# Kernel tuning notes

Hardware: AMD Instinct MI355X
Metric: run time of the kernel (lower is better)

Reference implementation:

```python
import jax, jax.numpy as jnp
import numpy as np
from jax import lax

MODEL_DIM = 384
KERNEL = 15
PAD = (KERNEL - 1) // 2
BATCH = 4096


def fake_quant(x, bits):
    """Per-tensor symmetric fake quantization with straight-through estimator.
    scale = max|x| / qmax, q = clip(round(x/scale), qmin, qmax), dq = q*scale.
    """
    qmax = float(2 ** (bits - 1) - 1)
    qmin = -float(2 ** (bits - 1))
    scale = jnp.maximum(jnp.max(jnp.abs(x)) / qmax, jnp.asarray(1e-8, x.dtype))
    dq = jnp.clip(jnp.round(x / scale), qmin, qmax) * scale
    return x + lax.stop_gradient(dq - x)  # STE: identity gradient


def setup_inputs() -> dict:
    key = jax.random.key(0)
    k = jax.random.split(key, 7)
    image = jax.random.normal(k[0], (BATCH, 28, 28), dtype=jnp.float32)
    # LinearQuant(28 -> model_dim)
    W1 = jax.random.normal(k[1], (MODEL_DIM, 28), dtype=jnp.float32) * (1.0 / np.sqrt(28))
    b1 = jax.random.normal(k[2], (MODEL_DIM,), dtype=jnp.float32) * 0.01
    # depthwise Conv1DQuant(model_dim, model_dim, K, groups=model_dim): weight [C_out, 1, K]
    Wc = jax.random.normal(k[3], (MODEL_DIM, 1, KERNEL), dtype=jnp.float32) * (1.0 / np.sqrt(KERNEL))
    bc = jax.random.normal(k[4], (MODEL_DIM,), dtype=jnp.float32) * 0.01
    # LinearQuant(28*model_dim -> 10)
    Wf = jax.random.normal(k[5], (10, 28 * MODEL_DIM), dtype=jnp.float32) * (1.0 / np.sqrt(28 * MODEL_DIM))
    bf = jax.random.normal(k[6], (10,), dtype=jnp.float32) * 0.01
    return {"image": image, "W1": W1, "b1": b1, "Wc": Wc, "bc": bc, "Wf": Wf, "bf": bf}


def reference(image, W1, b1, Wc, bc, Wf, bf):
    inp = image.reshape(-1, 28, 28)
    # linear_1 with 8-bit activation fake-quant in and 3-bit weight fake-quant
    x = fake_quant(inp, 8)
    lin = jnp.einsum('blf,of->blo', x, fake_quant(W1, 3)) + b1  # [B,28,model_dim]
    out1 = jnp.tanh(fake_quant(lin, 8))
    # depthwise conv1d over length 28, channels model_dim
    xc = jnp.transpose(fake_quant(out1, 8), (0, 2, 1))  # [B,C,L]
    conv = lax.conv_general_dilated(
        xc, fake_quant(Wc, 3), window_strides=(1,), padding=[(PAD, PAD)],
        dimension_numbers=('NCH', 'OIH', 'NCH'), feature_group_count=MODEL_DIM)
    conv = conv + bc[None, :, None]                      # [B,C,L]
    conv = jnp.transpose(conv, (0, 2, 1))                # [B,L,C]
    out2 = jnp.tanh(fake_quant(conv, 8)).reshape(-1, MODEL_DIM * 28)
    # final linear
    logits = fake_quant(out2, 8) @ fake_quant(Wf, 3).T + bf  # [B,10]
    return fake_quant(logits, 8)
```

## Files before the change

kernel.cpp:

```cpp
#include <hip/hip_runtime.h>

#define BATCH 4096
#define MD 384
#define KW 15
#define LSEQ 28
#define FIN 28
#define NX (BATCH*LSEQ*FIN)
#define NROWS (BATCH*LSEQ)

#define B_SCF  0
#define B_LUT1 256
#define B_LUT2 512
#define B_PT0  1024
#define B_PT1  33792
#define B_PT2  50176
#define B_PTL  66560
#define B_W1B  74752
#define B_WCQ  99328
#define B_WFB  105472
#define B_LG   277504
#define B_XQB  441344
#define B_CWG  7781376

typedef __bf16 bf16x8 __attribute__((ext_vector_type(8)));
typedef float f32x4 __attribute__((ext_vector_type(4)));
typedef int i32x4 __attribute__((ext_vector_type(4)));

#if __has_builtin(__builtin_amdgcn_sdot4)
#define SDOT4(a,b,c) __builtin_amdgcn_sdot4((a),(b),(c),false)
#else
__device__ __forceinline__ int SDOT4(int a,int b,int c){
  c += ((a<<24)>>24)*((b<<24)>>24);
  c += ((a<<16)>>24)*((b<<16)>>24);
  c += ((a<<8)>>24)*((b<<8)>>24);
  c += (a>>24)*(b>>24);
  return c;
}
#endif

#if __has_builtin(__builtin_amdgcn_alignbyte)
#define ALIGNB(hi,lo,s) __builtin_amdgcn_alignbyte((hi),(lo),(s))
#else
#define ALIGNB(hi,lo,s) ((int)(((unsigned)(lo)>>(8*(s)))|((unsigned)(hi)<<(32-8*(s)))))
#endif

__device__ __forceinline__ unsigned short f2bf(float f){
  return (unsigned short)(__float_as_uint(f)>>16);
}
__device__ __forceinline__ unsigned lut_bperm(int iw,int lutw){
  int res=__builtin_amdgcn_ds_bpermute(iw,lutw);
  return ((unsigned)res>>(8*(iw&3)))&0xFFu;
}

__device__ __forceinline__ void blkStore4(float m0,float m1,float m2,float m3,float4* dst){
  #pragma unroll
  for(int off=32;off;off>>=1){
    m0=fmaxf(m0,__shfl_xor(m0,off,64));
    m1=fmaxf(m1,__shfl_xor(m1,off,64));
    m2=fmaxf(m2,__shfl_xor(m2,off,64));
    m3=fmaxf(m3,__shfl_xor(m3,off,64));
  }
  __shared__ float sm[4][4];
  int wid=threadIdx.x>>6;
  if((threadIdx.x&63)==0){sm[wid][0]=m0;sm[wid][1]=m1;sm[wid][2]=m2;sm[wid][3]=m3;}
  __syncthreads();
  if(threadIdx.x==0){
    for(int i=1;i<4;i++){
      m0=fmaxf(m0,sm[i][0]);m1=fmaxf(m1,sm[i][1]);
      m2=fmaxf(m2,sm[i][2]);m3=fmaxf(m3,sm[i][3]);
    }
    *dst=make_float4(m0,m1,m2,m3);
  }
}

__device__ __forceinline__ void blkStoreMM(float mn,float mx,float2* dst){
  #pragma unroll
  for(int off=32;off;off>>=1){
    mn=fminf(mn,__shfl_xor(mn,off,64));
    mx=fmaxf(mx,__shfl_xor(mx,off,64));
  }
  __shared__ float smn[8],smx[8];
  int wid=threadIdx.x>>6, nw=blockDim.x>>6;
  if((threadIdx.x&63)==0){smn[wid]=mn;smx[wid]=mx;}
  __syncthreads();
  if(threadIdx.x==0){
    for(int i=1;i<nw;i++){mn=fminf(mn,smn[i]);mx=fmaxf(mx,smx[i]);}
    *dst=make_float2(mn,mx);
  }
}

__global__ __launch_bounds__(256)
void k_maxabs_in(const float* __restrict__ img,const float* __restrict__ W1,
                 const float* __restrict__ Wc,const float* __restrict__ Wf,
                 float4* __restrict__ pt0){
  float m0=0.f,m1=0.f,m2=0.f,m3=0.f;
  const int N4=NX/4;
  const int NW1=MD*FIN, NWC=MD*KW, NWF=10*MD*LSEQ;
  const int total=N4+NW1+NWC+NWF;
  const float4* img4=(const float4*)img;
  for(int i=blockIdx.x*blockDim.x+threadIdx.x;i<total;i+=gridDim.x*blockDim.x){
    if(i<N4){
      float4 v=img4[i];
      m0=fmaxf(m0,fmaxf(fmaxf(fabsf(v.x),fabsf(v.y)),fmaxf(fabsf(v.z),fabsf(v.w))));
    }
    else if(i<N4+NW1) m1=fmaxf(m1,fabsf(W1[i-N4]));
    else if(i<N4+NW1+NWC) m2=fmaxf(m2,fabsf(Wc[i-N4-NW1]));
    else m3=fmaxf(m3,fabsf(Wf[i-N4-NW1-NWC]));
  }
  blkStore4(m0,m1,m2,m3,&pt0[blockIdx.x]);
}

__global__ __launch_bounds__(256)
void k_prep(const float* __restrict__ img,const float* __restrict__ W1,
            const float* __restrict__ Wc,const float* __restrict__ Wf,
            const float4* __restrict__ pt0,float* __restrict__ scf,
            char* __restrict__ wsb){
  int t=threadIdx.x;
  float m0=0.f,m1=0.f,m2=0.f,m3=0.f;
  for(int i=t;i<2048;i+=256){
    float4 v=pt0[i];
    m0=fmaxf(m0,v.x);m1=fmaxf(m1,v.y);m2=fmaxf(m2,v.z);m3=fmaxf(m3,v.w);
  }
  #pragma unroll
  for(int off=32;off;off>>=1){
    m0=fmaxf(m0,__shfl_xor(m0,off,64));
    m1=fmaxf(m1,__shfl_xor(m1,off,64));
    m2=fmaxf(m2,__shfl_xor(m2,off,64));
    m3=fmaxf(m3,__shfl_xor(m3,off,64));
  }
  __shared__ float sm[4][4];
  __shared__ float bsv[4];
  int wid=t>>6;
  if((t&63)==0){sm[wid][0]=m0;sm[wid][1]=m1;sm[wid][2]=m2;sm[wid][3]=m3;}
  __syncthreads();
  if(t==0){
    for(int i=1;i<4;i++){
      m0=fmaxf(m0,sm[i][0]);m1=fmaxf(m1,sm[i][1]);
      m2=fmaxf(m2,sm[i][2]);m3=fmaxf(m3,sm[i][3]);
    }
    bsv[0]=fmaxf(m0/127.f,1e-8f);
    bsv[1]=fmaxf(m1/3.f,1e-8f);
    bsv[2]=fmaxf(m2/3.f,1e-8f);
    bsv[3]=fmaxf(m3/3.f,1e-8f);
    if(blockIdx.x==0){scf[0]=bsv[0];scf[1]=bsv[1];scf[2]=bsv[2];scf[3]=bsv[3];}
  }
  __syncthreads();
  float s_img=bsv[0], s_w1=bsv[1], s_wc=bsv[2], s_wf=bsv[3];
  float inv_img=1.f/s_img;
  unsigned short* xqb=(unsigned short*)(wsb+B_XQB);
  unsigned short* w1b=(unsigned short*)(wsb+B_W1B);
  char* wcpk=wsb+B_WCQ;
  char* wfb=wsb+B_WFB;
  const int T0=NROWS*32;
  const int T1=T0+MD*32;
  const int T2=T1+MD*16;
  const int T3=T2+10*10752;
  for(int i=blockIdx.x*blockDim.x+threadIdx.x;i<T3;i+=gridDim.x*blockDim.x){
    if(i<T0){
      int row=i>>5, cc=i&31;
      float q = cc<FIN ? fminf(fmaxf(rintf(img[row*FIN+cc]*inv_img),-128.f),127.f) : 0.f;
      xqb[i]=f2bf(q);
    } else if(i<T1){
      int j=i-T0; int o=j>>5, cc=j&31;
      float q = cc<FIN ? fminf(fmaxf(rintf(W1[o*FIN+cc]/s_w1),-4.f),3.f) : 0.f;
      w1b[j]=f2bf(q);
    } else if(i<T2){
      int j=i-T1; int c=j>>4, k=j&15;
      char q=0;
      if(k<KW) q=(char)(int)fminf(fmaxf(rintf(Wc[c*KW+k]/s_wc),-4.f),3.f);
      wcpk[j]=q;
    } else {
      int j=i-T2;
      int n=j/10752, r=j-n*10752;
      int c=r/28, l=r-c*28;
      wfb[j]=(char)(int)fminf(fmaxf(rintf(Wf[n*10752+l*MD+c]/s_wf),-4.f),3.f);
    }
  }
}

__global__ __launch_bounds__(256)
void k_redmm(const float2* __restrict__ pt,int n,float* __restrict__ scf,
             int preIdx,int outIdx,char* __restrict__ lutg){
  int t=threadIdx.x;
  float mn=1e30f,mx=-1e30f;
  for(int i=t;i<n;i+=256){
    float2 v=pt[i];
    mn=fminf(mn,v.x); mx=fmaxf(mx,v.y);
  }
  #pragma unroll
  for(int off=32;off;off>>=1){
    mn=fminf(mn,__shfl_xor(mn,off,64));
    mx=fmaxf(mx,__shfl_xor(mx,off,64));
  }
  __shared__ float smn[4],smx[4];
  __shared__ float bs,bso;
  int wid=t>>6;
  if((t&63)==0){smn[wid]=mn;smx[wid]=mx;}
  __syncthreads();
  if(t==0){
    for(int i=1;i<4;i++){mn=fminf(mn,smn[i]);mx=fmaxf(mx,smx[i]);}
    float ma=fmaxf(fabsf(mn),fabsf(mx));
    float s=fmaxf(ma/127.f,1e-8f);
    float a1=fabsf(fminf(fmaxf(rintf(mn/s),-128.f),127.f)*s);
    float a2=fabsf(fminf(fmaxf(rintf(mx/s),-128.f),127.f)*s);
    float so=fmaxf(tanhf(fmaxf(a1,a2))/127.f,1e-8f);
    scf[preIdx]=s; scf[outIdx]=so;
    bs=s; bso=so;
  }
  __syncthreads();
  float d=(float)(t-128)*bs;
  lutg[t]=(char)(int)fminf(fmaxf(rintf(tanhf(d)/bso),-128.f),127.f);
}

#define CWS 29
#define DWS 2692
template<int MODE>
__global__ __launch_bounds__(512)
void k_fused(const unsigned short* __restrict__ xqb,const unsigned short* __restrict__ w1b,
             const float* __restrict__ b1,const float* __restrict__ scf,
             const char* __restrict__ lut1g,const char* __restrict__ lut2g,
             const char* __restrict__ wcpk,const float* __restrict__ bc,
             const char* __restrict__ wfb,const float* __restrict__ bfv,
             int* __restrict__ cwg,
             float2* __restrict__ ptmm,float* __restrict__ lg,
             float* __restrict__ ptl){
  __shared__ int ldsI[MD*CWS];
  __shared__ int psumN[8][10][4];
  int t=threadIdx.x, wid=t>>6, lane=t&63, l4=lane>>4, l15=lane&15;

  bf16x8 bfr[3]; float b1v[3]; bf16x8 af[7];
  if constexpr(MODE<2){
    const int* src=(const int*)w1b;
    for(int i=t;i<6144;i+=512) ldsI[i]=src[i];
    __syncthreads();
    unsigned short* Wlds=(unsigned short*)ldsI;
    #pragma unroll
    for(int ni=0;ni<3;ni++){
      int o=(wid*3+ni)*16+l15;
      bfr[ni]=*(const bf16x8*)&Wlds[o*32+l4*8];
      b1v[ni]=b1[o];
    }
    int r0=blockIdx.x*112;
    #pragma unroll
    for(int mt=0;mt<7;mt++)
      af[mt]=*(const bf16x8*)&xqb[(size_t)(r0+mt*16+l15)*32+l4*8];
  } else {
    const int4* src=(const int4*)(cwg+(size_t)blockIdx.x*10752);
    for(int jj=t;jj<2688;jj+=512){
      int4 v=src[jj];
      int j=jj*4, o=j/28, idx=j-o*28, base=o*CWS+idx;
      ldsI[base]=v.x; ldsI[base+1]=v.y; ldsI[base+2]=v.z; ldsI[base+3]=v.w;
    }
  }

  float sg=scf[0]*scf[1];
  float sgi=sg, b1s[3]={0.f,0.f,0.f};
  int lutA_w=0,lutB_w=0;
  float ck1=1.f,inv_cv=1.f,sfac=1.f,gsc=1.f;
  if constexpr(MODE>=1){
    sfac=scf[5]*scf[2];
  }
  if constexpr(MODE==1){
    float inv_lin=1.f/scf[4];
    sgi=sg*inv_lin;
    #pragma unroll
    for(int ni=0;ni<3;ni++) b1s[ni]=fmaf(b1v[ni],inv_lin,128.f);
    lutA_w=((const int*)lut1g)[lane];
  }
  if constexpr(MODE==2){
    inv_cv=1.f/scf[6];
    ck1=sfac*inv_cv;
    gsc=scf[3]*scf[7];
    lutB_w=((const int*)lut2g)[lane];
  }
  if constexpr(MODE>=1) __syncthreads();

  if constexpr(MODE<2){
    f32x4 zero={0.f,0.f,0.f,0.f};
    float mnn[3]={1e30f,1e30f,1e30f},mxx[3]={-1e30f,-1e30f,-1e30f};
    #pragma unroll
    for(int ni=0;ni<3;ni++){
      int o=(wid*3+ni)*16+l15;
      #pragma unroll
      for(int mt=0;mt<7;mt++){
        f32x4 acc=__builtin_amdgcn_mfma_f32_16x16x32_bf16(af[mt],bfr[ni],zero,0,0,0);
        if constexpr(MODE==0){
          #pragma unroll
          for(int r=0;r<4;r++){
            mnn[ni]=fminf(mnn[ni],acc[r]); mxx[ni]=fmaxf(mxx[ni],acc[r]);
          }
        } else {
          unsigned w=0;
          #pragma unroll
          for(int r=0;r<4;r++){
            float x=fmaf(acc[r],sgi,b1s[ni]);
            int iw=(int)__builtin_amdgcn_fmed3f(rintf(x),0.f,255.f);
            w|=lut_bperm(iw,lutA_w)<<(8*r);
          }
          ldsI[o*CWS+mt*4+l4]=(int)w;
        }
      }
    }
    if constexpr(MODE==0){
      float mn=1e30f,mx=-1e30f;
      #pragma unroll
      for(int ni=0;ni<3;ni++){
        mn=fminf(mn,fmaf(mnn[ni],sg,b1v[ni]));
        mx=fmaxf(mx,fmaf(mxx[ni],sg,b1v[ni]));
      }
      blkStoreMM(mn,mx,&ptmm[blockIdx.x]);
      return;
    }
    __syncthreads();
    {
      int4* dst=(int4*)(cwg+(size_t)blockIdx.x*10752);
      for(int jj=t;jj<2688;jj+=512){
        int j=jj*4, o=j/28, idx=j-o*28, base=o*CWS+idx;
        int4 v; v.x=ldsI[base]; v.y=ldsI[base+1]; v.z=ldsI[base+2]; v.w=ldsI[base+3];
        dst[jj]=v;
      }
    }
  }

  int oww[3][7];
  float mnc=1e30f,mxc=-1e30f;
  #pragma unroll
  for(int rr=0;rr<3;rr++){
    int j=t+rr*512;
    int s=j/384, c=j-s*384;
    i32x4 wq=*(const i32x4*)(wcpk+(size_t)c*16);
    float cbias=bc[c];
    float cq2=0.f;
    if constexpr(MODE==2) cq2=fmaf(cbias,inv_cv,128.f);
    int ext[11];
    ext[0]=0; ext[1]=0; ext[9]=0; ext[10]=0;
    #pragma unroll
    for(int i=0;i<7;i++) ext[2+i]=ldsI[c*CWS+s*7+i];
    int imn=0x7FFFFFFF,imx=0x80000000;
    #pragma unroll
    for(int l=0;l<LSEQ;l++){
      const int eb=l+1, bi=eb>>2, sh=eb&3;
      int A0,A1,A2,A3;
      if(sh==0){A0=ext[bi];A1=ext[bi+1];A2=ext[bi+2];A3=ext[bi+3];}
      else{
        A0=ALIGNB(ext[bi+1],ext[bi],sh);
        A1=ALIGNB(ext[bi+2],ext[bi+1],sh);
        A2=ALIGNB(ext[bi+3],ext[bi+2],sh);
        A3=ALIGNB(ext[bi+4],ext[bi+3],sh);
      }
      int idot=SDOT4(A0,wq[0],SDOT4(A1,wq[1],SDOT4(A2,wq[2],SDOT4(A3,wq[3],0))));
      if constexpr(MODE==1){
        imn=min(imn,idot); imx=max(imx,idot);
      } else {
        float x=fmaf((float)idot,ck1,cq2);
        int iw=(int)__builtin_amdgcn_fmed3f(rintf(x),0.f,255.f);
        unsigned q2=lut_bperm(iw,lutB_w);
        if((l&3)==0) oww[rr][l>>2]=(int)q2;
        else oww[rr][l>>2]|=(int)(q2<<(8*(l&3)));
      }
    }
    if constexpr(MODE==1){
      mnc=fminf(mnc,fmaf((float)imn,sfac,cbias));
      mxc=fmaxf(mxc,fmaf((float)imx,sfac,cbias));
    }
  }
  if constexpr(MODE==1){
    blkStoreMM(mnc,mxc,&ptmm[blockIdx.x]);
    return;
  }

  __syncthreads();
  #pragma unroll
  for(int rr=0;rr<3;rr++){
    int j=t+rr*512;
    int s=j/384, c=j-s*384;
    #pragma unroll
    for(int i=0;i<7;i++) ldsI[s*DWS+c*7+i]=oww[rr][i];
  }
  __syncthreads();

  {
    i32x4 acc0={0,0,0,0}, acc1={0,0,0,0};
    const char* ldsB=(const char*)ldsI;
    for(int kb=wid;kb<168;kb+=16){
      i32x4 a=*(const i32x4*)(ldsB+(size_t)(l15&3)*(DWS*4)+kb*64+l4*16);
      i32x4 b=*(const i32x4*)(wfb+(size_t)l15*10752+kb*64+l4*16);
      acc0=__builtin_amdgcn_mfma_i32_16x16x64_i8(a,b,acc0,0,0,0);
      int kb2=kb+8;
      if(kb2<168){
        i32x4 a2=*(const i32x4*)(ldsB+(size_t)(l15&3)*(DWS*4)+kb2*64+l4*16);
        i32x4 b2=*(const i32x4*)(wfb+(size_t)l15*10752+kb2*64+l4*16);
        acc1=__builtin_amdgcn_mfma_i32_16x16x64_i8(a2,b2,acc1,0,0,0);
      }
    }
    if(l4==0&&l15<10){
      #pragma unroll
      for(int r=0;r<4;r++) psumN[wid][l15][r]=acc0[r]+acc1[r];
    }
  }
  __syncthreads();
  float m=0.f;
  if(t<40){
    int s=t/10, o=t-s*10;
    int sum=0;
    #pragma unroll
    for(int w=0;w<8;w++) sum+=psumN[w][o][s];
    float v=fmaf((float)sum,gsc,bfv[o]);
    lg[(blockIdx.x*4+s)*10+o]=v;
    m=fabsf(v);
  }
  if(t<64){
    #pragma unroll
    for(int off=32;off;off>>=1) m=fmaxf(m,__shfl_xor(m,off,64));
    if(t==0) ptl[blockIdx.x]=m;
  }
}

__global__ __launch_bounds__(256)
void k_final(const float* __restrict__ lg,const float* __restrict__ ptl,
             float* __restrict__ out){
  int t=threadIdx.x;
  float m=0.f;
  for(int i=t;i<1024;i+=256) m=fmaxf(m,ptl[i]);
  #pragma unroll
  for(int off=32;off;off>>=1) m=fmaxf(m,__shfl_xor(m,off,64));
  __shared__ float sm[4];
  __shared__ float sv;
  int wid=t>>6;
  if((t&63)==0) sm[wid]=m;
  __syncthreads();
  if(t==0){
    for(int k=1;k<4;k++) m=fmaxf(m,sm[k]);
    sv=fmaxf(m/127.f,1e-8f);
  }
  __syncthreads();
  float s=sv;
  int i=blockIdx.x*256+t;
  out[i]=fminf(fmaxf(rintf(lg[i]/s),-128.f),127.f)*s;
}

extern "C" void kernel_launch(void* const* d_in, const int* in_sizes, int n_in,
                              void* d_out, int out_size, void* d_ws, size_t ws_size,
                              hipStream_t stream){
  const float* img=(const float*)d_in[0];
  const float* W1 =(const float*)d_in[1];
  const float* b1 =(const float*)d_in[2];
  const float* Wc =(const float*)d_in[3];
  const float* bc =(const float*)d_in[4];
  const float* Wf =(const float*)d_in[5];
  const float* bf =(const float*)d_in[6];
  float* out=(float*)d_out;
  char* wsb=(char*)d_ws;
  float* scf=(float*)(wsb+B_SCF);
  float4* pt0=(float4*)(wsb+B_PT0);
  float2* pt1=(float2*)(wsb+B_PT1);
  float2* pt2=(float2*)(wsb+B_PT2);
  float* ptl=(float*)(wsb+B_PTL);
  float* lg=(float*)(wsb+B_LG);
  int* cwg=(int*)(wsb+B_CWG);
  const unsigned short* xqb=(const unsigned short*)(wsb+B_XQB);
  const unsigned short* w1b=(const unsigned short*)(wsb+B_W1B);
  const char* wcpk=wsb+B_WCQ;
  const char* wfb=wsb+B_WFB;

  k_maxabs_in<<<2048,256,0,stream>>>(img,W1,Wc,Wf,pt0);
  k_prep<<<2048,256,0,stream>>>(img,W1,Wc,Wf,pt0,scf,wsb);
  k_fused<0><<<1024,512,0,stream>>>(xqb,w1b,b1,scf,nullptr,nullptr,wcpk,bc,wfb,bf,cwg,pt1,nullptr,nullptr);
  k_redmm<<<1,256,0,stream>>>(pt1,1024,scf,4,5,wsb+B_LUT1);
  k_fused<1><<<1024,512,0,stream>>>(xqb,w1b,b1,scf,wsb+B_LUT1,nullptr,wcpk,bc,wfb,bf,cwg,pt2,nullptr,nullptr);
  k_redmm<<<1,256,0,stream>>>(pt2,1024,scf,6,7,wsb+B_LUT2);
  k_fused<2><<<1024,512,0,stream>>>(xqb,w1b,b1,scf,wsb+B_LUT1,wsb+B_LUT2,wcpk,bc,wfb,bf,cwg,nullptr,lg,ptl);
  k_final<<<160,256,0,stream>>>(lg,ptl,out);
}
```

Measured before the change: 105.8 us.

## Merge all stages into one cooperative persistent kernel with grid syncs

Replaces the eight separate launches (maxabs, prep, three fused passes, two reductions, final) with a single cooperative kernel. Grid-wide barriers separate the stages, each block loops over tiles persistently, and the scale reductions and tanh lookup tables are recomputed per block in shared memory. This removes launch gaps and the single-block reduction kernels. In exchange the grid is capped at co-resident blocks (at most 512), each block processes multiple tiles serially, and each grid sync costs a global barrier.

```diff
diff --git a/kernel.cpp b/kernel.cpp
--- a/kernel.cpp
+++ b/kernel.cpp
@@ -1,4 +1,6 @@
 #include <hip/hip_runtime.h>
+#include <hip/hip_cooperative_groups.h>
+namespace cg = cooperative_groups;
 
 #define BATCH 4096
 #define MD 384
@@ -7,10 +9,8 @@
 #define FIN 28
 #define NX (BATCH*LSEQ*FIN)
 #define NROWS (BATCH*LSEQ)
-
-#define B_SCF  0
-#define B_LUT1 256
-#define B_LUT2 512
+#define NTILE 1024
+
 #define B_PT0  1024
 #define B_PT1  33792
 #define B_PT2  50176
@@ -52,184 +52,131 @@
   return ((unsigned)res>>(8*(iw&3)))&0xFFu;
 }
 
-__device__ __forceinline__ void blkStore4(float m0,float m1,float m2,float m3,float4* dst){
-  #pragma unroll
-  for(int off=32;off;off>>=1){
-    m0=fmaxf(m0,__shfl_xor(m0,off,64));
-    m1=fmaxf(m1,__shfl_xor(m1,off,64));
-    m2=fmaxf(m2,__shfl_xor(m2,off,64));
-    m3=fmaxf(m3,__shfl_xor(m3,off,64));
-  }
-  __shared__ float sm[4][4];
-  int wid=threadIdx.x>>6;
-  if((threadIdx.x&63)==0){sm[wid][0]=m0;sm[wid][1]=m1;sm[wid][2]=m2;sm[wid][3]=m3;}
-  __syncthreads();
-  if(threadIdx.x==0){
-    for(int i=1;i<4;i++){
-      m0=fmaxf(m0,sm[i][0]);m1=fmaxf(m1,sm[i][1]);
-      m2=fmaxf(m2,sm[i][2]);m3=fmaxf(m3,sm[i][3]);
-    }
-    *dst=make_float4(m0,m1,m2,m3);
-  }
-}
-
-__device__ __forceinline__ void blkStoreMM(float mn,float mx,float2* dst){
-  #pragma unroll
-  for(int off=32;off;off>>=1){
-    mn=fminf(mn,__shfl_xor(mn,off,64));
-    mx=fmaxf(mx,__shfl_xor(mx,off,64));
-  }
-  __shared__ float smn[8],smx[8];
-  int wid=threadIdx.x>>6, nw=blockDim.x>>6;
-  if((threadIdx.x&63)==0){smn[wid]=mn;smx[wid]=mx;}
-  __syncthreads();
-  if(threadIdx.x==0){
-    for(int i=1;i<nw;i++){mn=fminf(mn,smn[i]);mx=fmaxf(mx,smx[i]);}
-    *dst=make_float2(mn,mx);
-  }
-}
-
-__global__ __launch_bounds__(256)
-void k_maxabs_in(const float* __restrict__ img,const float* __restrict__ W1,
-                 const float* __restrict__ Wc,const float* __restrict__ Wf,
-                 float4* __restrict__ pt0){
-  float m0=0.f,m1=0.f,m2=0.f,m3=0.f;
-  const int N4=NX/4;
-  const int NW1=MD*FIN, NWC=MD*KW, NWF=10*MD*LSEQ;
-  const int total=N4+NW1+NWC+NWF;
-  const float4* img4=(const float4*)img;
-  for(int i=blockIdx.x*blockDim.x+threadIdx.x;i<total;i+=gridDim.x*blockDim.x){
-    if(i<N4){
-      float4 v=img4[i];
-      m0=fmaxf(m0,fmaxf(fmaxf(fabsf(v.x),fabsf(v.y)),fmaxf(fabsf(v.z),fabsf(v.w))));
-    }
-    else if(i<N4+NW1) m1=fmaxf(m1,fabsf(W1[i-N4]));
-    else if(i<N4+NW1+NWC) m2=fmaxf(m2,fabsf(Wc[i-N4-NW1]));
-    else m3=fmaxf(m3,fabsf(Wf[i-N4-NW1-NWC]));
-  }
-  blkStore4(m0,m1,m2,m3,&pt0[blockIdx.x]);
-}
-
-__global__ __launch_bounds__(256)
-void k_prep(const float* __restrict__ img,const float* __restrict__ W1,
-            const float* __restrict__ Wc,const float* __restrict__ Wf,
-            const float4* __restrict__ pt0,float* __restrict__ scf,
-            char* __restrict__ wsb){
-  int t=threadIdx.x;
-  float m0=0.f,m1=0.f,m2=0.f,m3=0.f;
-  for(int i=t;i<2048;i+=256){
-    float4 v=pt0[i];
-    m0=fmaxf(m0,v.x);m1=fmaxf(m1,v.y);m2=fmaxf(m2,v.z);m3=fmaxf(m3,v.w);
-  }
-  #pragma unroll
-  for(int off=32;off;off>>=1){
-    m0=fmaxf(m0,__shfl_xor(m0,off,64));
-    m1=fmaxf(m1,__shfl_xor(m1,off,64));
-    m2=fmaxf(m2,__shfl_xor(m2,off,64));
-    m3=fmaxf(m3,__shfl_xor(m3,off,64));
-  }
-  __shared__ float sm[4][4];
-  __shared__ float bsv[4];
-  int wid=t>>6;
-  if((t&63)==0){sm[wid][0]=m0;sm[wid][1]=m1;sm[wid][2]=m2;sm[wid][3]=m3;}
-  __syncthreads();
-  if(t==0){
-    for(int i=1;i<4;i++){
-      m0=fmaxf(m0,sm[i][0]);m1=fmaxf(m1,sm[i][1]);
-      m2=fmaxf(m2,sm[i][2]);m3=fmaxf(m3,sm[i][3]);
-    }
-    bsv[0]=fmaxf(m0/127.f,1e-8f);
-    bsv[1]=fmaxf(m1/3.f,1e-8f);
-    bsv[2]=fmaxf(m2/3.f,1e-8f);
-    bsv[3]=fmaxf(m3/3.f,1e-8f);
-    if(blockIdx.x==0){scf[0]=bsv[0];scf[1]=bsv[1];scf[2]=bsv[2];scf[3]=bsv[3];}
-  }
-  __syncthreads();
-  float s_img=bsv[0], s_w1=bsv[1], s_wc=bsv[2], s_wf=bsv[3];
-  float inv_img=1.f/s_img;
+#define CWS 29
+#define DWS 2692
+
+__global__ __launch_bounds__(512,4)
+void k_mega(const float* __restrict__ img,const float* __restrict__ W1v,
+            const float* __restrict__ b1,const float* __restrict__ Wc,
+            const float* __restrict__ bc,const float* __restrict__ Wf,
+            const float* __restrict__ bfv,float* __restrict__ out,
+            char* __restrict__ wsb,int nblk){
+  cg::grid_group grid=cg::this_grid();
+  __shared__ int ldsI[MD*CWS];
+  __shared__ int psumN[8][10][4];
+  __shared__ char lutA[256];
+  __shared__ char lutB[256];
+  __shared__ float sred[8][4];
+  __shared__ float bsv[9];
+
+  int t=threadIdx.x, bid=blockIdx.x;
+  int wid=t>>6, lane=t&63, l4=lane>>4, l15=lane&15;
+
+  float4* pt0=(float4*)(wsb+B_PT0);
+  float2* pt1=(float2*)(wsb+B_PT1);
+  float2* pt2=(float2*)(wsb+B_PT2);
+  float* ptl=(float*)(wsb+B_PTL);
+  float* lg=(float*)(wsb+B_LG);
+  int* cwg=(int*)(wsb+B_CWG);
   unsigned short* xqb=(unsigned short*)(wsb+B_XQB);
   unsigned short* w1b=(unsigned short*)(wsb+B_W1B);
   char* wcpk=wsb+B_WCQ;
   char* wfb=wsb+B_WFB;
-  const int T0=NROWS*32;
-  const int T1=T0+MD*32;
-  const int T2=T1+MD*16;
-  const int T3=T2+10*10752;
-  for(int i=blockIdx.x*blockDim.x+threadIdx.x;i<T3;i+=gridDim.x*blockDim.x){
-    if(i<T0){
-      int row=i>>5, cc=i&31;
-      float q = cc<FIN ? fminf(fmaxf(rintf(img[row*FIN+cc]*inv_img),-128.f),127.f) : 0.f;
-      xqb[i]=f2bf(q);
-    } else if(i<T1){
-      int j=i-T0; int o=j>>5, cc=j&31;
-      float q = cc<FIN ? fminf(fmaxf(rintf(W1[o*FIN+cc]/s_w1),-4.f),3.f) : 0.f;
-      w1b[j]=f2bf(q);
-    } else if(i<T2){
-      int j=i-T1; int c=j>>4, k=j&15;
-      char q=0;
-      if(k<KW) q=(char)(int)fminf(fmaxf(rintf(Wc[c*KW+k]/s_wc),-4.f),3.f);
-      wcpk[j]=q;
-    } else {
-      int j=i-T2;
-      int n=j/10752, r=j-n*10752;
-      int c=r/28, l=r-c*28;
-      wfb[j]=(char)(int)fminf(fmaxf(rintf(Wf[n*10752+l*MD+c]/s_wf),-4.f),3.f);
-    }
-  }
-}
-
-__global__ __launch_bounds__(256)
-void k_redmm(const float2* __restrict__ pt,int n,float* __restrict__ scf,
-             int preIdx,int outIdx,char* __restrict__ lutg){
-  int t=threadIdx.x;
-  float mn=1e30f,mx=-1e30f;
-  for(int i=t;i<n;i+=256){
-    float2 v=pt[i];
-    mn=fminf(mn,v.x); mx=fmaxf(mx,v.y);
-  }
-  #pragma unroll
-  for(int off=32;off;off>>=1){
-    mn=fminf(mn,__shfl_xor(mn,off,64));
-    mx=fmaxf(mx,__shfl_xor(mx,off,64));
-  }
-  __shared__ float smn[4],smx[4];
-  __shared__ float bs,bso;
-  int wid=t>>6;
-  if((t&63)==0){smn[wid]=mn;smx[wid]=mx;}
-  __syncthreads();
-  if(t==0){
-    for(int i=1;i<4;i++){mn=fminf(mn,smn[i]);mx=fmaxf(mx,smx[i]);}
-    float ma=fmaxf(fabsf(mn),fabsf(mx));
-    float s=fmaxf(ma/127.f,1e-8f);
-    float a1=fabsf(fminf(fmaxf(rintf(mn/s),-128.f),127.f)*s);
-    float a2=fabsf(fminf(fmaxf(rintf(mx/s),-128.f),127.f)*s);
-    float so=fmaxf(tanhf(fmaxf(a1,a2))/127.f,1e-8f);
-    scf[preIdx]=s; scf[outIdx]=so;
-    bs=s; bso=so;
-  }
-  __syncthreads();
-  float d=(float)(t-128)*bs;
-  lutg[t]=(char)(int)fminf(fmaxf(rintf(tanhf(d)/bso),-128.f),127.f);
-}
-
-#define CWS 29
-#define DWS 2692
-template<int MODE>
-__global__ __launch_bounds__(512)
-void k_fused(const unsigned short* __restrict__ xqb,const unsigned short* __restrict__ w1b,
-             const float* __restrict__ b1,const float* __restrict__ scf,
-             const char* __restrict__ lut1g,const char* __restrict__ lut2g,
-             const char* __restrict__ wcpk,const float* __restrict__ bc,
-             const char* __restrict__ wfb,const float* __restrict__ bfv,
-             int* __restrict__ cwg,
-             float2* __restrict__ ptmm,float* __restrict__ lg,
-             float* __restrict__ ptl){
-  __shared__ int ldsI[MD*CWS];
-  __shared__ int psumN[8][10][4];
-  int t=threadIdx.x, wid=t>>6, lane=t&63, l4=lane>>4, l15=lane&15;
-
-  bf16x8 bfr[3]; float b1v[3]; bf16x8 af[7];
-  if constexpr(MODE<2){
+
+  {
+    float m0=0.f,m1=0.f,m2=0.f,m3=0.f;
+    const int N4=NX/4;
+    const int NW1=MD*FIN,NWC=MD*KW,NWF=10*MD*LSEQ;
+    const int total=N4+NW1+NWC+NWF;
+    const float4* img4=(const float4*)img;
+    for(int i=bid*512+t;i<total;i+=nblk*512){
+      if(i<N4){
+        float4 v=img4[i];
+        m0=fmaxf(m0,fmaxf(fmaxf(fabsf(v.x),fabsf(v.y)),fmaxf(fabsf(v.z),fabsf(v.w))));
+      }
+      else if(i<N4+NW1) m1=fmaxf(m1,fabsf(W1v[i-N4]));
+      else if(i<N4+NW1+NWC) m2=fmaxf(m2,fabsf(Wc[i-N4-NW1]));
+      else m3=fmaxf(m3,fabsf(Wf[i-N4-NW1-NWC]));
+    }
+    #pragma unroll
+    for(int off=32;off;off>>=1){
+      m0=fmaxf(m0,__shfl_xor(m0,off,64));
+      m1=fmaxf(m1,__shfl_xor(m1,off,64));
+      m2=fmaxf(m2,__shfl_xor(m2,off,64));
+      m3=fmaxf(m3,__shfl_xor(m3,off,64));
+    }
+    if(lane==0){sred[wid][0]=m0;sred[wid][1]=m1;sred[wid][2]=m2;sred[wid][3]=m3;}
+    __syncthreads();
+    if(t==0){
+      for(int i=1;i<8;i++){
+        m0=fmaxf(m0,sred[i][0]);m1=fmaxf(m1,sred[i][1]);
+        m2=fmaxf(m2,sred[i][2]);m3=fmaxf(m3,sred[i][3]);
+      }
+      pt0[bid]=make_float4(m0,m1,m2,m3);
+    }
+    __syncthreads();
+  }
+  grid.sync();
+  {
+    float m0=0.f,m1=0.f,m2=0.f,m3=0.f;
+    for(int i=t;i<nblk;i+=512){
+      float4 v=pt0[i];
+      m0=fmaxf(m0,v.x);m1=fmaxf(m1,v.y);m2=fmaxf(m2,v.z);m3=fmaxf(m3,v.w);
+    }
+    #pragma unroll
+    for(int off=32;off;off>>=1){
+      m0=fmaxf(m0,__shfl_xor(m0,off,64));
+      m1=fmaxf(m1,__shfl_xor(m1,off,64));
+      m2=fmaxf(m2,__shfl_xor(m2,off,64));
+      m3=fmaxf(m3,__shfl_xor(m3,off,64));
+    }
+    if(lane==0){sred[wid][0]=m0;sred[wid][1]=m1;sred[wid][2]=m2;sred[wid][3]=m3;}
+    __syncthreads();
+    if(t==0){
+      for(int i=1;i<8;i++){
+        m0=fmaxf(m0,sred[i][0]);m1=fmaxf(m1,sred[i][1]);
+        m2=fmaxf(m2,sred[i][2]);m3=fmaxf(m3,sred[i][3]);
+      }
+      bsv[0]=fmaxf(m0/127.f,1e-8f);
+      bsv[1]=fmaxf(m1/3.f,1e-8f);
+      bsv[2]=fmaxf(m2/3.f,1e-8f);
+      bsv[3]=fmaxf(m3/3.f,1e-8f);
+    }
+    __syncthreads();
+  }
+  {
+    float s_img=bsv[0],s_w1=bsv[1],s_wc=bsv[2],s_wf=bsv[3];
+    float inv_img=1.f/s_img;
+    const int T0=NROWS*32;
+    const int T1=T0+MD*32;
+    const int T2=T1+MD*16;
+    const int T3=T2+10*10752;
+    for(int i=bid*512+t;i<T3;i+=nblk*512){
+      if(i<T0){
+        int row=i>>5, cc=i&31;
+        float q = cc<FIN ? fminf(fmaxf(rintf(img[row*FIN+cc]*inv_img),-128.f),127.f) : 0.f;
+        xqb[i]=f2bf(q);
+      } else if(i<T1){
+        int j=i-T0; int o=j>>5, cc=j&31;
+        float q = cc<FIN ? fminf(fmaxf(rintf(W1v[o*FIN+cc]/s_w1),-4.f),3.f) : 0.f;
+        w1b[j]=f2bf(q);
+      } else if(i<T2){
+        int j=i-T1; int c=j>>4, k=j&15;
+        char q=0;
+        if(k<KW) q=(char)(int)fminf(fmaxf(rintf(Wc[c*KW+k]/s_wc),-4.f),3.f);
+        wcpk[j]=q;
+      } else {
+        int j=i-T2;
+        int n=j/10752, r=j-n*10752;
+        int c=r/28, l=r-c*28;
+        wfb[j]=(char)(int)fminf(fmaxf(rintf(Wf[n*10752+l*MD+c]/s_wf),-4.f),3.f);
+      }
+    }
+  }
+  grid.sync();
+
+  bf16x8 bfr[3]; float b1v[3];
+  {
     const int* src=(const int*)w1b;
     for(int i=t;i<6144;i+=512) ldsI[i]=src[i];
     __syncthreads();
@@ -240,56 +187,100 @@
       bfr[ni]=*(const bf16x8*)&Wlds[o*32+l4*8];
       b1v[ni]=b1[o];
     }
-    int r0=blockIdx.x*112;
-    #pragma unroll
-    for(int mt=0;mt<7;mt++)
-      af[mt]=*(const bf16x8*)&xqb[(size_t)(r0+mt*16+l15)*32+l4*8];
-  } else {
-    const int4* src=(const int4*)(cwg+(size_t)blockIdx.x*10752);
-    for(int jj=t;jj<2688;jj+=512){
-      int4 v=src[jj];
-      int j=jj*4, o=j/28, idx=j-o*28, base=o*CWS+idx;
-      ldsI[base]=v.x; ldsI[base+1]=v.y; ldsI[base+2]=v.z; ldsI[base+3]=v.w;
-    }
-  }
-
-  float sg=scf[0]*scf[1];
-  float sgi=sg, b1s[3]={0.f,0.f,0.f};
-  int lutA_w=0,lutB_w=0;
-  float ck1=1.f,inv_cv=1.f,sfac=1.f,gsc=1.f;
-  if constexpr(MODE>=1){
-    sfac=scf[5]*scf[2];
-  }
-  if constexpr(MODE==1){
-    float inv_lin=1.f/scf[4];
-    sgi=sg*inv_lin;
-    #pragma unroll
-    for(int ni=0;ni<3;ni++) b1s[ni]=fmaf(b1v[ni],inv_lin,128.f);
-    lutA_w=((const int*)lut1g)[lane];
-  }
-  if constexpr(MODE==2){
-    inv_cv=1.f/scf[6];
-    ck1=sfac*inv_cv;
-    gsc=scf[3]*scf[7];
-    lutB_w=((const int*)lut2g)[lane];
-  }
-  if constexpr(MODE>=1) __syncthreads();
-
-  if constexpr(MODE<2){
+    float sg=bsv[0]*bsv[1];
     f32x4 zero={0.f,0.f,0.f,0.f};
     float mnn[3]={1e30f,1e30f,1e30f},mxx[3]={-1e30f,-1e30f,-1e30f};
-    #pragma unroll
-    for(int ni=0;ni<3;ni++){
-      int o=(wid*3+ni)*16+l15;
-      #pragma unroll
-      for(int mt=0;mt<7;mt++){
-        f32x4 acc=__builtin_amdgcn_mfma_f32_16x16x32_bf16(af[mt],bfr[ni],zero,0,0,0);
-        if constexpr(MODE==0){
+    for(int tile=bid;tile<NTILE;tile+=nblk){
+      bf16x8 af[7];
+      int r0=tile*112;
+      #pragma unroll
+      for(int mt=0;mt<7;mt++)
+        af[mt]=*(const bf16x8*)&xqb[(size_t)(r0+mt*16+l15)*32+l4*8];
+      #pragma unroll
+      for(int ni=0;ni<3;ni++){
+        #pragma unroll
+        for(int mt=0;mt<7;mt++){
+          f32x4 acc=__builtin_amdgcn_mfma_f32_16x16x32_bf16(af[mt],bfr[ni],zero,0,0,0);
           #pragma unroll
           for(int r=0;r<4;r++){
             mnn[ni]=fminf(mnn[ni],acc[r]); mxx[ni]=fmaxf(mxx[ni],acc[r]);
           }
-        } else {
+        }
+      }
+    }
+    float mn=1e30f,mx=-1e30f;
+    #pragma unroll
+    for(int ni=0;ni<3;ni++){
+      mn=fminf(mn,fmaf(mnn[ni],sg,b1v[ni]));
+      mx=fmaxf(mx,fmaf(mxx[ni],sg,b1v[ni]));
+    }
+    #pragma unroll
+    for(int off=32;off;off>>=1){
+      mn=fminf(mn,__shfl_xor(mn,off,64));
+      mx=fmaxf(mx,__shfl_xor(mx,off,64));
+    }
+    if(lane==0){sred[wid][0]=mn;sred[wid][1]=mx;}
+    __syncthreads();
+    if(t==0){
+      for(int i=1;i<8;i++){mn=fminf(mn,sred[i][0]);mx=fmaxf(mx,sred[i][1]);}
+      pt1[bid]=make_float2(mn,mx);
+    }
+    __syncthreads();
+  }
+  grid.sync();
+  {
+    float mn=1e30f,mx=-1e30f;
+    for(int i=t;i<nblk;i+=512){
+      float2 v=pt1[i]; mn=fminf(mn,v.x); mx=fmaxf(mx,v.y);
+    }
+    #pragma unroll
+    for(int off=32;off;off>>=1){
+      mn=fminf(mn,__shfl_xor(mn,off,64));
+      mx=fmaxf(mx,__shfl_xor(mx,off,64));
+    }
+    if(lane==0){sred[wid][0]=mn;sred[wid][1]=mx;}
+    __syncthreads();
+    if(t==0){
+      for(int i=1;i<8;i++){mn=fminf(mn,sred[i][0]);mx=fmaxf(mx,sred[i][1]);}
+      float ma=fmaxf(fabsf(mn),fabsf(mx));
+      float s=fmaxf(ma/127.f,1e-8f);
+      float a1=fabsf(fminf(fmaxf(rintf(mn/s),-128.f),127.f)*s);
+      float a2=fabsf(fminf(fmaxf(rintf(mx/s),-128.f),127.f)*s);
+      bsv[4]=s;
+      bsv[5]=fmaxf(tanhf(fmaxf(a1,a2))/127.f,1e-8f);
+    }
+    __syncthreads();
+    if(t<256){
+      float d=(float)(t-128)*bsv[4];
+      lutA[t]=(char)(int)fminf(fmaxf(rintf(tanhf(d)/bsv[5]),-128.f),127.f);
+    }
+    __syncthreads();
+  }
+
+  {
+    float sg=bsv[0]*bsv[1];
+    float inv_lin=1.f/bsv[4];
+    float sgi=sg*inv_lin;
+    float b1s[3];
+    #pragma unroll
+    for(int ni=0;ni<3;ni++) b1s[ni]=fmaf(b1v[ni],inv_lin,128.f);
+    int lutA_w=((const int*)lutA)[lane];
+    float sfac=bsv[5]*bsv[2];
+    f32x4 zero={0.f,0.f,0.f,0.f};
+    float mnc=1e30f,mxc=-1e30f;
+    for(int tile=bid;tile<NTILE;tile+=nblk){
+      __syncthreads();
+      bf16x8 af[7];
+      int r0=tile*112;
+      #pragma unroll
+      for(int mt=0;mt<7;mt++)
+        af[mt]=*(const bf16x8*)&xqb[(size_t)(r0+mt*16+l15)*32+l4*8];
+      #pragma unroll
+      for(int ni=0;ni<3;ni++){
+        int o=(wid*3+ni)*16+l15;
+        #pragma unroll
+        for(int mt=0;mt<7;mt++){
+          f32x4 acc=__builtin_amdgcn_mfma_f32_16x16x32_bf16(af[mt],bfr[ni],zero,0,0,0);
           unsigned w=0;
           #pragma unroll
           for(int r=0;r<4;r++){
@@ -300,143 +291,200 @@
           ldsI[o*CWS+mt*4+l4]=(int)w;
         }
       }
-    }
-    if constexpr(MODE==0){
-      float mn=1e30f,mx=-1e30f;
-      #pragma unroll
-      for(int ni=0;ni<3;ni++){
-        mn=fminf(mn,fmaf(mnn[ni],sg,b1v[ni]));
-        mx=fmaxf(mx,fmaf(mxx[ni],sg,b1v[ni]));
-      }
-      blkStoreMM(mn,mx,&ptmm[blockIdx.x]);
-      return;
-    }
-    __syncthreads();
-    {
-      int4* dst=(int4*)(cwg+(size_t)blockIdx.x*10752);
-      for(int jj=t;jj<2688;jj+=512){
-        int j=jj*4, o=j/28, idx=j-o*28, base=o*CWS+idx;
-        int4 v; v.x=ldsI[base]; v.y=ldsI[base+1]; v.z=ldsI[base+2]; v.w=ldsI[base+3];
-        dst[jj]=v;
-      }
-    }
-  }
-
-  int oww[3][7];
-  float mnc=1e30f,mxc=-1e30f;
-  #pragma unroll
-  for(int rr=0;rr<3;rr++){
-    int j=t+rr*512;
-    int s=j/384, c=j-s*384;
-    i32x4 wq=*(const i32x4*)(wcpk+(size_t)c*16);
-    float cbias=bc[c];
-    float cq2=0.f;
-    if constexpr(MODE==2) cq2=fmaf(cbias,inv_cv,128.f);
-    int ext[11];
-    ext[0]=0; ext[1]=0; ext[9]=0; ext[10]=0;
-    #pragma unroll
-    for(int i=0;i<7;i++) ext[2+i]=ldsI[c*CWS+s*7+i];
-    int imn=0x7FFFFFFF,imx=0x80000000;
-    #pragma unroll
-    for(int l=0;l<LSEQ;l++){
-      const int eb=l+1, bi=eb>>2, sh=eb&3;
-      int A0,A1,A2,A3;
-      if(sh==0){A0=ext[bi];A1=ext[bi+1];A2=ext[bi+2];A3=ext[bi+3];}
-      else{
-        A0=ALIGNB(ext[bi+1],ext[bi],sh);
-        A1=ALIGNB(ext[bi+2],ext[bi+1],sh);
-        A2=ALIGNB(ext[bi+3],ext[bi+2],sh);
-        A3=ALIGNB(ext[bi+4],ext[bi+3],sh);
-      }
-      int idot=SDOT4(A0,wq[0],SDOT4(A1,wq[1],SDOT4(A2,wq[2],SDOT4(A3,wq[3],0))));
-      if constexpr(MODE==1){
-        imn=min(imn,idot); imx=max(imx,idot);
-      } else {
-        float x=fmaf((float)idot,ck1,cq2);
-        int iw=(int)__builtin_amdgcn_fmed3f(rintf(x),0.f,255.f);
-        unsigned q2=lut_bperm(iw,lutB_w);
-        if((l&3)==0) oww[rr][l>>2]=(int)q2;
-        else oww[rr][l>>2]|=(int)(q2<<(8*(l&3)));
-      }
-    }
-    if constexpr(MODE==1){
-      mnc=fminf(mnc,fmaf((float)imn,sfac,cbias));
-      mxc=fmaxf(mxc,fmaf((float)imx,sfac,cbias));
-    }
-  }
-  if constexpr(MODE==1){
-    blkStoreMM(mnc,mxc,&ptmm[blockIdx.x]);
-    return;
-  }
-
-  __syncthreads();
-  #pragma unroll
-  for(int rr=0;rr<3;rr++){
-    int j=t+rr*512;
-    int s=j/384, c=j-s*384;
-    #pragma unroll
-    for(int i=0;i<7;i++) ldsI[s*DWS+c*7+i]=oww[rr][i];
-  }
-  __syncthreads();
-
-  {
-    i32x4 acc0={0,0,0,0}, acc1={0,0,0,0};
-    const char* ldsB=(const char*)ldsI;
-    for(int kb=wid;kb<168;kb+=16){
-      i32x4 a=*(const i32x4*)(ldsB+(size_t)(l15&3)*(DWS*4)+kb*64+l4*16);
-      i32x4 b=*(const i32x4*)(wfb+(size_t)l15*10752+kb*64+l4*16);
-      acc0=__builtin_amdgcn_mfma_i32_16x16x64_i8(a,b,acc0,0,0,0);
-      int kb2=kb+8;
-      if(kb2<168){
-        i32x4 a2=*(const i32x4*)(ldsB+(size_t)(l15&3)*(DWS*4)+kb2*64+l4*16);
-        i32x4 b2=*(const i32x4*)(wfb+(size_t)l15*10752+kb2*64+l4*16);
-        acc1=__builtin_amdgcn_mfma_i32_16x16x64_i8(a2,b2,acc1,0,0,0);
-      }
-    }
-    if(l4==0&&l15<10){
-      #pragma unroll
-      for(int r=0;r<4;r++) psumN[wid][l15][r]=acc0[r]+acc1[r];
-    }
-  }
-  __syncthreads();
-  float m=0.f;
-  if(t<40){
-    int s=t/10, o=t-s*10;
-    int sum=0;
-    #pragma unroll
-    for(int w=0;w<8;w++) sum+=psumN[w][o][s];
-    float v=fmaf((float)sum,gsc,bfv[o]);
-    lg[(blockIdx.x*4+s)*10+o]=v;
-    m=fabsf(v);
-  }
-  if(t<64){
+      __syncthreads();
+      {
+        int4* dst=(int4*)(cwg+(size_t)tile*10752);
+        for(int jj=t;jj<2688;jj+=512){
+          int j=jj*4, o=j/28, idx=j-o*28, base=o*CWS+idx;
+          int4 v; v.x=ldsI[base]; v.y=ldsI[base+1]; v.z=ldsI[base+2]; v.w=ldsI[base+3];
+          dst[jj]=v;
+        }
+      }
+      #pragma unroll
+      for(int rr=0;rr<3;rr++){
+        int j=t+rr*512;
+        int s=j/384, c=j-s*384;
+        i32x4 wq=*(const i32x4*)(wcpk+(size_t)c*16);
+        float cbias=bc[c];
+        int ext[11];
+        ext[0]=0; ext[1]=0; ext[9]=0; ext[10]=0;
+        #pragma unroll
+        for(int i=0;i<7;i++) ext[2+i]=ldsI[c*CWS+s*7+i];
+        int imn=0x7FFFFFFF,imx=0x80000000;
+        #pragma unroll
+        for(int l=0;l<LSEQ;l++){
+          const int eb=l+1, bi=eb>>2, sh=eb&3;
+          int A0,A1,A2,A3;
+          if(sh==0){A0=ext[bi];A1=ext[bi+1];A2=ext[bi+2];A3=ext[bi+3];}
+          else{
+            A0=ALIGNB(ext[bi+1],ext[bi],sh);
+            A1=ALIGNB(ext[bi+2],ext[bi+1],sh);
+            A2=ALIGNB(ext[bi+3],ext[bi+2],sh);
+            A3=ALIGNB(ext[bi+4],ext[bi+3],sh);
+          }
+          int idot=SDOT4(A0,wq[0],SDOT4(A1,wq[1],SDOT4(A2,wq[2],SDOT4(A3,wq[3],0))));
+          imn=min(imn,idot); imx=max(imx,idot);
+        }
+        mnc=fminf(mnc,fmaf((float)imn,sfac,cbias));
+        mxc=fmaxf(mxc,fmaf((float)imx,sfac,cbias));
+      }
+    }
+    #pragma unroll
+    for(int off=32;off;off>>=1){
+      mnc=fminf(mnc,__shfl_xor(mnc,off,64));
+      mxc=fmaxf(mxc,__shfl_xor(mxc,off,64));
+    }
+    __syncthreads();
+    if(lane==0){sred[wid][0]=mnc;sred[wid][1]=mxc;}
+    __syncthreads();
+    if(t==0){
+      for(int i=1;i<8;i++){mnc=fminf(mnc,sred[i][0]);mxc=fmaxf(mxc,sred[i][1]);}
+      pt2[bid]=make_float2(mnc,mxc);
+    }
+    __syncthreads();
+  }
+  grid.sync();
+  {
+    float mn=1e30f,mx=-1e30f;
+    for(int i=t;i<nblk;i+=512){
+      float2 v=pt2[i]; mn=fminf(mn,v.x); mx=fmaxf(mx,v.y);
+    }
+    #pragma unroll
+    for(int off=32;off;off>>=1){
+      mn=fminf(mn,__shfl_xor(mn,off,64));
+      mx=fmaxf(mx,__shfl_xor(mx,off,64));
+    }
+    if(lane==0){sred[wid][0]=mn;sred[wid][1]=mx;}
+    __syncthreads();
+    if(t==0){
+      for(int i=1;i<8;i++){mn=fminf(mn,sred[i][0]);mx=fmaxf(mx,sred[i][1]);}
+      float ma=fmaxf(fabsf(mn),fabsf(mx));
+      float s=fmaxf(ma/127.f,1e-8f);
+      float a1=fabsf(fminf(fmaxf(rintf(mn/s),-128.f),127.f)*s);
+      float a2=fabsf(fminf(fmaxf(rintf(mx/s),-128.f),127.f)*s);
+      bsv[6]=s;
+      bsv[7]=fmaxf(tanhf(fmaxf(a1,a2))/127.f,1e-8f);
+    }
+    __syncthreads();
+    if(t<256){
+      float d=(float)(t-128)*bsv[6];
+      lutB[t]=(char)(int)fminf(fmaxf(rintf(tanhf(d)/bsv[7]),-128.f),127.f);
+    }
+    __syncthreads();
+  }
+
+  {
+    float inv_cv=1.f/bsv[6];
+    float ck1=bsv[5]*bsv[2]*inv_cv;
+    float gsc=bsv[3]*bsv[7];
+    int lutB_w=((const int*)lutB)[lane];
+    float mL=0.f;
+    for(int tile=bid;tile<NTILE;tile+=nblk){
+      __syncthreads();
+      {
+        const int4* src=(const int4*)(cwg+(size_t)tile*10752);
+        for(int jj=t;jj<2688;jj+=512){
+          int4 v=src[jj];
+          int j=jj*4, o=j/28, idx=j-o*28, base=o*CWS+idx;
+          ldsI[base]=v.x; ldsI[base+1]=v.y; ldsI[base+2]=v.z; ldsI[base+3]=v.w;
+        }
+      }
+      __syncthreads();
+      int oww[3][7];
+      #pragma unroll
+      for(int rr=0;rr<3;rr++){
+        int j=t+rr*512;
+        int s=j/384, c=j-s*384;
+        i32x4 wq=*(const i32x4*)(wcpk+(size_t)c*16);
+        float cq2=fmaf(bc[c],inv_cv,128.f);
+        int ext[11];
+        ext[0]=0; ext[1]=0; ext[9]=0; ext[10]=0;
+        #pragma unroll
+        for(int i=0;i<7;i++) ext[2+i]=ldsI[c*CWS+s*7+i];
+        #pragma unroll
+        for(int l=0;l<LSEQ;l++){
+          const int eb=l+1, bi=eb>>2, sh=eb&3;
+          int A0,A1,A2,A3;
+          if(sh==0){A0=ext[bi];A1=ext[bi+1];A2=ext[bi+2];A3=ext[bi+3];}
+          else{
+            A0=ALIGNB(ext[bi+1],ext[bi],sh);
+            A1=ALIGNB(ext[bi+2],ext[bi+1],sh);
+            A2=ALIGNB(ext[bi+3],ext[bi+2],sh);
+            A3=ALIGNB(ext[bi+4],ext[bi+3],sh);
+          }
+          int idot=SDOT4(A0,wq[0],SDOT4(A1,wq[1],SDOT4(A2,wq[2],SDOT4(A3,wq[3],0))));
+          float x=fmaf((float)idot,ck1,cq2);
+          int iw=(int)__builtin_amdgcn_fmed3f(rintf(x),0.f,255.f);
+          unsigned q2=lut_bperm(iw,lutB_w);
+          if((l&3)==0) oww[rr][l>>2]=(int)q2;
+          else oww[rr][l>>2]|=(int)(q2<<(8*(l&3)));
+        }
+      }
+      __syncthreads();
+      #pragma unroll
+      for(int rr=0;rr<3;rr++){
+        int j=t+rr*512;
+        int s=j/384, c=j-s*384;
+        #pragma unroll
+        for(int i=0;i<7;i++) ldsI[s*DWS+c*7+i]=oww[rr][i];
+      }
+      __syncthreads();
+      {
+        i32x4 acc0={0,0,0,0}, acc1={0,0,0,0};
+        const char* ldsB=(const char*)ldsI;
+        for(int kb=wid;kb<168;kb+=16){
+          i32x4 a=*(const i32x4*)(ldsB+(size_t)(l15&3)*(DWS*4)+kb*64+l4*16);
+          i32x4 b=*(const i32x4*)(wfb+(size_t)l15*10752+kb*64+l4*16);
+          acc0=__builtin_amdgcn_mfma_i32_16x16x64_i8(a,b,acc0,0,0,0);
+          int kb2=kb+8;
+          if(kb2<168){
+            i32x4 a2=*(const i32x4*)(ldsB+(size_t)(l15&3)*(DWS*4)+kb2*64+l4*16);
+            i32x4 b2=*(const i32x4*)(wfb+(size_t)l15*10752+kb2*64+l4*16);
+            acc1=__builtin_amdgcn_mfma_i32_16x16x64_i8(a2,b2,acc1,0,0,0);
+          }
+        }
+        if(l4==0&&l15<10){
+          #pragma unroll
+          for(int r=0;r<4;r++) psumN[wid][l15][r]=acc0[r]+acc1[r];
+        }
+      }
+      __syncthreads();
+      float m=0.f;
+      if(t<40){
+        int s=t/10, o=t-s*10;
+        int sum=0;
+        #pragma unroll
+        for(int w=0;w<8;w++) sum+=psumN[w][o][s];
+        float v=fmaf((float)sum,gsc,bfv[o]);
+        lg[(size_t)tile*40+t]=v;
+        m=fabsf(v);
+      }
+      if(t<64){
+        #pragma unroll
+        for(int off=32;off;off>>=1) m=fmaxf(m,__shfl_xor(m,off,64));
+        if(t==0) mL=fmaxf(mL,m);
+      }
+    }
+    if(t==0) ptl[bid]=mL;
+    __syncthreads();
+  }
+  grid.sync();
+  {
+    float m=0.f;
+    for(int i=t;i<nblk;i+=512) m=fmaxf(m,ptl[i]);
     #pragma unroll
     for(int off=32;off;off>>=1) m=fmaxf(m,__shfl_xor(m,off,64));
-    if(t==0) ptl[blockIdx.x]=m;
-  }
-}
-
-__global__ __launch_bounds__(256)
-void k_final(const float* __restrict__ lg,const float* __restrict__ ptl,
-             float* __restrict__ out){
-  int t=threadIdx.x;
-  float m=0.f;
-  for(int i=t;i<1024;i+=256) m=fmaxf(m,ptl[i]);
-  #pragma unroll
-  for(int off=32;off;off>>=1) m=fmaxf(m,__shfl_xor(m,off,64));
-  __shared__ float sm[4];
-  __shared__ float sv;
-  int wid=t>>6;
-  if((t&63)==0) sm[wid]=m;
-  __syncthreads();
-  if(t==0){
-    for(int k=1;k<4;k++) m=fmaxf(m,sm[k]);
-    sv=fmaxf(m/127.f,1e-8f);
-  }
-  __syncthreads();
-  float s=sv;
-  int i=blockIdx.x*256+t;
-  out[i]=fminf(fmaxf(rintf(lg[i]/s),-128.f),127.f)*s;
+    if(lane==0) sred[wid][0]=m;
+    __syncthreads();
+    if(t==0){
+      for(int i=1;i<8;i++) m=fmaxf(m,sred[i][0]);
+      bsv[8]=fmaxf(m/127.f,1e-8f);
+    }
+    __syncthreads();
+    float s=bsv[8];
+    for(int i=bid*512+t;i<BATCH*10;i+=nblk*512)
+      out[i]=fminf(fmaxf(rintf(lg[i]/s),-128.f),127.f)*s;
+  }
 }
 
 extern "C" void kernel_launch(void* const* d_in, const int* in_sizes, int n_in,
@@ -451,24 +499,21 @@
   const float* bf =(const float*)d_in[6];
   float* out=(float*)d_out;
   char* wsb=(char*)d_ws;
-  float* scf=(float*)(wsb+B_SCF);
-  float4* pt0=(float4*)(wsb+B_PT0);
-  float2* pt1=(float2*)(wsb+B_PT1);
-  float2* pt2=(float2*)(wsb+B_PT2);
-  float* ptl=(float*)(wsb+B_PTL);
-  float* lg=(float*)(wsb+B_LG);
-  int* cwg=(int*)(wsb+B_CWG);
-  const unsigned short* xqb=(const unsigned short*)(wsb+B_XQB);
-  const unsigned short* w1b=(const unsigned short*)(wsb+B_W1B);
-  const char* wcpk=wsb+B_WCQ;
-  const char* wfb=wsb+B_WFB;
-
-  k_maxabs_in<<<2048,256,0,stream>>>(img,W1,Wc,Wf,pt0);
-  k_prep<<<2048,256,0,stream>>>(img,W1,Wc,Wf,pt0,scf,wsb);
-  k_fused<0><<<1024,512,0,stream>>>(xqb,w1b,b1,scf,nullptr,nullptr,wcpk,bc,wfb,bf,cwg,pt1,nullptr,nullptr);
-  k_redmm<<<1,256,0,stream>>>(pt1,1024,scf,4,5,wsb+B_LUT1);
-  k_fused<1><<<1024,512,0,stream>>>(xqb,w1b,b1,scf,wsb+B_LUT1,nullptr,wcpk,bc,wfb,bf,cwg,pt2,nullptr,nullptr);
-  k_redmm<<<1,256,0,stream>>>(pt2,1024,scf,6,7,wsb+B_LUT2);
-  k_fused<2><<<1024,512,0,stream>>>(xqb,w1b,b1,scf,wsb+B_LUT1,wsb+B_LUT2,wcpk,bc,wfb,bf,cwg,nullptr,lg,ptl);
-  k_final<<<160,256,0,stream>>>(lg,ptl,out);
+
+  int nblk=512;
+  int maxb=0;
+  if(hipOccupancyMaxActiveBlocksPerMultiprocessor(&maxb,k_mega,512,0)==hipSuccess && maxb>0){
+    int dev=0; hipGetDevice(&dev);
+    int cus=0;
+    if(hipDeviceGetAttribute(&cus,hipDeviceAttributeMultiprocessorCount,dev)==hipSuccess && cus>0){
+      int cap=maxb*cus;
+      if(cap<nblk) nblk=cap;
+    }
+  } else {
+    nblk=256;
+  }
+
+  void* args[]={(void*)&img,(void*)&W1,(void*)&b1,(void*)&Wc,(void*)&bc,
+                (void*)&Wf,(void*)&bf,(void*)&out,(void*)&wsb,(void*)&nblk};
+  hipLaunchCooperativeKernel((void*)k_mega,dim3(nblk),dim3(512),args,0,stream);
 }
```

After: 259.9 us. 146% more time.
